# Optimization experiments

Hardware: AMD Instinct MI355X
Metric: run time of the kernel (lower is better)

Reference implementation:

```python
import jax, jax.numpy as jnp
import numpy as np

B, C, H, W = 16, 64, 128, 128
C8 = C // 8


def setup_inputs() -> dict:
    key = jax.random.key(0)
    ks = jax.random.split(key, 8)
    s = 0.05
    return {
        "x": jax.random.normal(ks[0], (B, C, H, W), dtype=jnp.float32),
        "Wq": jax.random.normal(ks[1], (C8, C), dtype=jnp.float32) * s,
        "bq": jax.random.normal(ks[2], (C8,), dtype=jnp.float32) * s,
        "Wk": jax.random.normal(ks[3], (C8, C), dtype=jnp.float32) * s,
        "bk": jax.random.normal(ks[4], (C8,), dtype=jnp.float32) * s,
        "Wv": jax.random.normal(ks[5], (C, C), dtype=jnp.float32) * s,
        "bv": jax.random.normal(ks[6], (C,), dtype=jnp.float32) * s,
        "gamma": jnp.zeros((1,), dtype=jnp.float32),
    }


def _criss_cross(x, Wq, bq, Wk, bk, Wv, bv, gamma):
    # 1x1 convs == channel-mixing matmuls
    q = jnp.einsum("bchw,oc->bohw", x, Wq) + bq[None, :, None, None]  # [B,C8,H,W]
    k = jnp.einsum("bchw,oc->bohw", x, Wk) + bk[None, :, None, None]  # [B,C8,H,W]
    v = jnp.einsum("bchw,oc->bohw", x, Wv) + bv[None, :, None, None]  # [B,C,H,W]

    h = x.shape[2]
    # column (H-axis) attention scores; diagonal masked to -inf
    energy_H = jnp.einsum("bchw,bciw->bhwi", q, k)  # [B,H,W,H]
    diag = jnp.eye(h, dtype=bool)[None, :, None, :]  # mask where query row == key row
    energy_H = jnp.where(diag, -jnp.inf, energy_H)
    # row (W-axis) attention scores
    energy_W = jnp.einsum("bchw,bchj->bhwj", q, k)  # [B,H,W,W]

    # joint softmax over concatenated H+W axis
    att = jax.nn.softmax(jnp.concatenate([energy_H, energy_W], axis=3), axis=3)
    att_H = att[:, :, :, :h]    # [B,H,W,H]
    att_W = att[:, :, :, h:]    # [B,H,W,W]

    out_H = jnp.einsum("bhwi,bciw->bchw", att_H, v)
    out_W = jnp.einsum("bhwj,bchj->bchw", att_W, v)
    return gamma[0] * (out_H + out_W) + x


def reference(x, Wq, bq, Wk, bk, Wv, bv, gamma):
    return _criss_cross(x, Wq, bq, Wk, bk, Wv, bv, gamma)
```

## Files before the change

kernel.cpp:

```cpp
#include <hip/hip_runtime.h>

#define HW 128
#define CC 64
#define C8V 8
#define NB 16
#define LOG2E 1.44269504088896f

typedef _Float16 h1;
typedef _Float16 h2 __attribute__((ext_vector_type(2)));
typedef _Float16 half8 __attribute__((ext_vector_type(8)));
typedef float float16v __attribute__((ext_vector_type(16)));
typedef uint uv4 __attribute__((ext_vector_type(4)));

__device__ __forceinline__ uint packh2(float a, float b) {
#if __has_builtin(__builtin_amdgcn_cvt_pkrtz)
  return __builtin_bit_cast(uint, __builtin_amdgcn_cvt_pkrtz(a, b));
#else
  h2 v; v[0] = (h1)a; v[1] = (h1)b; return __builtin_bit_cast(uint, v);
#endif
}
__device__ __forceinline__ ushort f2h(float a) { h1 v = (h1)a; return __builtin_bit_cast(ushort, v); }
__device__ __forceinline__ float  h2f(ushort a) { return (float)__builtin_bit_cast(h1, a); }

__device__ __forceinline__ float fexp2(float x) {
#if __has_builtin(__builtin_amdgcn_exp2f)
  return __builtin_amdgcn_exp2f(x);
#else
  return exp2f(x);
#endif
}

__device__ __forceinline__ float16v mfma16(uv4 a, uv4 b, float16v c) {
  return __builtin_amdgcn_mfma_f32_32x32x16_f16(
      __builtin_bit_cast(half8, a), __builtin_bit_cast(half8, b), c, 0, 0, 0);
}

__global__ __launch_bounds__(256) void k_proj(
    const float* __restrict__ x,
    const float* __restrict__ Wq, const float* __restrict__ bq,
    const float* __restrict__ Wk, const float* __restrict__ bk,
    const float* __restrict__ Wv, const float* __restrict__ bv,
    ushort* __restrict__ q, ushort* __restrict__ k,
    ushort* __restrict__ qT, ushort* __restrict__ kT,
    ushort* __restrict__ v)
{
  alignas(16) __shared__ ushort smem[16128];
  __shared__ float bias_l[96];
  ushort* x_l = smem;
  ushort* W_l = smem + 128 * 72;

  int t = threadIdx.x;
  int lane = t & 63, wv = t >> 6;
  int b = blockIdx.x >> 7, r = blockIdx.x & 127;

  #pragma unroll
  for (int i = 0; i < 20; ++i) {
    int idx = t + 256 * i; int o_ = idx >> 6, c = idx & 63;
    float wval = (o_ < 8) ? Wq[o_ * 64 + c] : (o_ < 16) ? Wk[(o_ - 8) * 64 + c] : Wv[(o_ - 16) * 64 + c];
    W_l[o_ * 72 + c] = f2h(wval);
  }
  if (t < 96) bias_l[t] = (t < 8) ? bq[t] : (t < 16) ? bk[t - 8] : (t < 80) ? bv[t - 16] : 0.f;

  const float* xrow = x + (size_t)(b * CC) * (HW * HW) + (size_t)r * HW;
  #pragma unroll
  for (int i = 0; i < 8; ++i) {
    int idx = t + 256 * i; int c = idx >> 5, w4 = idx & 31;
    float4 xv = *(const float4*)(xrow + (size_t)c * (HW * HW) + w4 * 4);
    x_l[(w4 * 4 + 0) * 72 + c] = f2h(xv.x);
    x_l[(w4 * 4 + 1) * 72 + c] = f2h(xv.y);
    x_l[(w4 * 4 + 2) * 72 + c] = f2h(xv.z);
    x_l[(w4 * 4 + 3) * 72 + c] = f2h(xv.w);
  }
  __syncthreads();

  int w = 32 * wv + (lane & 31);
  float16v acc0 = {}, acc1 = {}, acc2 = {};
  #pragma unroll
  for (int ks = 0; ks < 4; ++ks) {
    int c0 = 8 * (lane >> 5) + 16 * ks;
    uv4 Bx = *(const uv4*)&x_l[w * 72 + c0];
    uv4 a0 = *(const uv4*)&W_l[((lane & 31) + 0) * 72 + c0];
    uv4 a1 = *(const uv4*)&W_l[((lane & 31) + 32) * 72 + c0];
    uv4 a2 = *(const uv4*)&W_l[((lane & 31) + 64) * 72 + c0];
    acc0 = mfma16(a0, Bx, acc0);
    acc1 = mfma16(a1, Bx, acc1);
    acc2 = mfma16(a2, Bx, acc2);
  }
  __syncthreads();

  ushort* o_l  = smem;
  ushort* qk_l = smem + 8192;
  int hi = lane >> 5;

  {
    int zw = t >> 1, sel = t & 1;
    *(uv4*)&qk_l[zw * 40 + 8 + 16 * sel] = (uv4){0, 0, 0, 0};
  }

  #pragma unroll
  for (int reg = 0; reg < 16; ++reg) {
    int orow = (reg & 3) + 8 * (reg >> 2) + 4 * hi;
    float v0 = acc0[reg] + bias_l[orow];
    if (orow < 8)       qk_l[w * 40 + orow] = f2h(v0 * LOG2E);
    else if (orow < 16) qk_l[w * 40 + 8 + orow] = f2h(v0);
    else                o_l[(orow - 16) * 128 + w] = f2h(v0);
    o_l[(orow + 16) * 128 + w] = f2h(acc1[reg] + bias_l[orow + 32]);
    if (orow < 16)
      o_l[(orow + 48) * 128 + w] = f2h(acc2[reg] + bias_l[orow + 64]);
  }
  __syncthreads();

  size_t pixbase = (size_t)(b * HW + r) * HW * 16;
  {
    int pw = t >> 1, part = t & 1;
    *(uv4*)(q + pixbase + t * 8) = *(const uv4*)&qk_l[pw * 40 + part * 8];
    *(uv4*)(k + pixbase + t * 8) = *(const uv4*)&qk_l[pw * 40 + 16 + part * 8];
    size_t tbase = ((size_t)(b * HW + pw) * HW + r) * 16 + part * 8;
    *(uv4*)(qT + tbase) = *(const uv4*)&qk_l[pw * 40 + part * 8];
    *(uv4*)(kT + tbase) = *(const uv4*)&qk_l[pw * 40 + 16 + part * 8];
  }
  ushort* vb = v + (size_t)(b * CC) * (HW * HW) + (size_t)r * HW;
  #pragma unroll
  for (int i = 0; i < 4; ++i) {
    int idx = t + 256 * i; int o_ = idx >> 4, w8 = idx & 15;
    *(uv4*)(vb + (size_t)o_ * (HW * HW) + w8 * 8) = *(const uv4*)&o_l[o_ * 128 + w8 * 8];
  }
}

__global__ __launch_bounds__(256) void k_transpose_v(const ushort* __restrict__ v,
                                                     ushort* __restrict__ vT)
{
  __shared__ ushort tl[128 * 130];
  int t = threadIdx.x;
  size_t base = (size_t)blockIdx.x * (HW * HW);
  const uint* ip = (const uint*)(v + base);
  uint* op = (uint*)(vT + base);
  int c2 = t & 63;
  int r0 = t >> 6;
  for (int it = 0; it < 32; ++it) {
    int r = it * 4 + r0;
    uint val = ip[r * 64 + c2];
    *(uint*)&tl[r * 130 + c2 * 2] = val;
  }
  __syncthreads();
  for (int it = 0; it < 32; ++it) {
    int wcol = it * 4 + r0;
    int hh = c2 * 2;
    uint lo = tl[hh * 130 + wcol];
    uint hi = tl[(hh + 1) * 130 + wcol];
    op[wcol * 64 + c2] = lo | (hi << 16);
  }
}

__global__ __launch_bounds__(256, 4) void k_attn_both(
    const ushort* __restrict__ qn, const ushort* __restrict__ kn,
    const ushort* __restrict__ qT, const ushort* __restrict__ kT,
    const ushort* __restrict__ vn, const ushort* __restrict__ vT,
    ushort* __restrict__ oW_, float* __restrict__ mW_, float* __restrict__ sW_,
    ushort* __restrict__ oH_, float* __restrict__ mH_, float* __restrict__ sH_)
{
  alignas(16) __shared__ uint V_l[64 * 64];

  int t = threadIdx.x;
  int lane = t & 63, wv = t >> 6;
  int hi = lane >> 5;
  int bid = blockIdx.x & 2047;
  bool maskf = blockIdx.x >= 2048;
  const ushort* qp = maskf ? qT : qn;
  const ushort* kp = maskf ? kT : kn;
  const ushort* vp = maskf ? vT : vn;
  ushort* op = maskf ? oH_ : oW_;
  float* mo = maskf ? mH_ : mW_;
  float* so = maskf ? sH_ : sW_;

  int b = bid >> 7, r = bid & 127;
  size_t plane32 = (size_t)(HW * HW) / 2;
  size_t pixbase = (size_t)(b * HW + r) * HW * 16;

  int qg = 32 * wv + (lane & 31);
  uv4 Bq = *(const uv4*)(qp + pixbase + (size_t)qg * 16 + hi * 8);
  uv4 ka[4];
  #pragma unroll
  for (int mt = 0; mt < 4; ++mt)
    ka[mt] = *(const uv4*)(kp + pixbase + (size_t)((lane & 31) + 32 * mt) * 16 + hi * 8);

  const uint* vrow = (const uint*)vp + (size_t)(b * CC) * plane32 + (size_t)r * 64;
  #pragma unroll
  for (int i = 0; i < 4; ++i) {
    int idx = t + 256 * i; int c = idx >> 4, j4 = idx & 15;
    uv4 val = *(const uv4*)(vrow + (size_t)c * plane32 + 4 * j4);
    uint byteoff = c * 256 + ((16 * j4) ^ ((c & 15) << 4));
    *(uv4*)((char*)V_l + byteoff) = val;
  }
  __syncthreads();

  float16v e[4];
  #pragma unroll
  for (int mt = 0; mt < 4; ++mt) {
    float16v z = {};
    e[mt] = mfma16(ka[mt], Bq, z);
  }

  if (maskf) {
    #pragma unroll
    for (int mt = 0; mt < 4; ++mt)
      #pragma unroll
      for (int reg = 0; reg < 16; ++reg) {
        int key = 32 * mt + ((reg & 3) + 8 * (reg >> 2) + 4 * hi);
        e[mt][reg] = (key == qg) ? -INFINITY : e[mt][reg];
      }
  }

  float m = -INFINITY;
  #pragma unroll
  for (int mt = 0; mt < 4; ++mt)
    #pragma unroll
    for (int reg = 0; reg < 16; reg += 2)
      m = fmaxf(m, fmaxf(e[mt][reg], e[mt][reg + 1]));
  m = fmaxf(m, __shfl_xor(m, 32));

  float s0 = 0.f, s1 = 0.f, s2 = 0.f, s3 = 0.f;
  #pragma unroll
  for (int mt = 0; mt < 4; ++mt) {
    #pragma unroll
    for (int reg = 0; reg < 16; reg += 4) {
      float p0 = fexp2(e[mt][reg + 0] - m);
      float p1 = fexp2(e[mt][reg + 1] - m);
      float p2 = fexp2(e[mt][reg + 2] - m);
      float p3 = fexp2(e[mt][reg + 3] - m);
      e[mt][reg + 0] = p0; e[mt][reg + 1] = p1;
      e[mt][reg + 2] = p2; e[mt][reg + 3] = p3;
      s0 += p0; s1 += p1; s2 += p2; s3 += p3;
    }
  }
  float s = (s0 + s1) + (s2 + s3);
  s += __shfl_xor(s, 32);
  if (lane < 32) {
    mo[(size_t)bid * HW + qg] = m;
    so[(size_t)bid * HW + qg] = s;
  }

  float16v acc0 = {}, acc1 = {};
  #pragma unroll
  for (int s8 = 0; s8 < 8; ++s8) {
    int mt = s8 >> 1, hf = s8 & 1;
    float p0 = e[mt][8 * hf + 0], p1 = e[mt][8 * hf + 1];
    float p2 = e[mt][8 * hf + 2], p3 = e[mt][8 * hf + 3];
    float p4 = e[mt][8 * hf + 4], p5 = e[mt][8 * hf + 5];
    float p6 = e[mt][8 * hf + 6], p7 = e[mt][8 * hf + 7];
    uint X = packh2(p0, p1), Y = packh2(p2, p3), Z = packh2(p4, p5), Wp = packh2(p6, p7);
    uint Xs = __shfl_xor(X, 32), Ys = __shfl_xor(Y, 32);
    uint Zs = __shfl_xor(Z, 32), Ws = __shfl_xor(Wp, 32);
    uv4 Bp;
    Bp[0] = (hi == 0) ? X  : Zs;
    Bp[1] = (hi == 0) ? Y  : Ws;
    Bp[2] = (hi == 0) ? Xs : Z;
    Bp[3] = (hi == 0) ? Ys : Wp;
    #pragma unroll
    for (int ct = 0; ct < 2; ++ct) {
      int c = (lane & 31) + 32 * ct;
      uint byteoff = c * 256 + ((16 * (hi + 2 * s8)) ^ ((c & 15) << 4));
      uv4 va = *(const uv4*)((const char*)V_l + byteoff);
      if (ct == 0) acc0 = mfma16(va, Bp, acc0);
      else         acc1 = mfma16(va, Bp, acc1);
    }
  }

  __syncthreads();
  ushort* o_l = (ushort*)V_l;
  int w = 32 * wv + (lane & 31);
  #pragma unroll
  for (int reg = 0; reg < 16; ++reg) {
    int c = (reg & 3) + 8 * (reg >> 2) + 4 * hi;
    o_l[(c +  0) * 128 + w] = f2h(acc0[reg]);
    o_l[(c + 32) * 128 + w] = f2h(acc1[reg]);
  }
  __syncthreads();
  ushort* ob = op + (size_t)(b * CC) * (HW * HW) + (size_t)r * HW;
  #pragma unroll
  for (int i = 0; i < 4; ++i) {
    int idx = t + 256 * i; int c = idx >> 4, w8 = idx & 15;
    *(uv4*)(ob + (size_t)c * (HW * HW) + w8 * 8) = *(const uv4*)&o_l[c * 128 + w8 * 8];
  }
}

__global__ __launch_bounds__(256) void k_alpha(
    const float* __restrict__ mH, const float* __restrict__ sH,
    const float* __restrict__ mW, const float* __restrict__ sW,
    ushort* __restrict__ aHT, ushort* __restrict__ aWn)
{
  __shared__ float mw_l[128 * 9], sw_l[128 * 9];
  __shared__ ushort aw_l[128 * 10];
  int t = threadIdx.x;
  int b = blockIdx.x >> 4, ws = blockIdx.x & 15;
  int w0 = ws * 8;
  const int PL = HW * HW;

  #pragma unroll
  for (int i = 0; i < 4; ++i) {
    int p = t + 256 * i;
    int w = p & 7, h = p >> 3;
    mw_l[h * 9 + w] = mW[(size_t)b * PL + h * HW + w0 + w];
    sw_l[h * 9 + w] = sW[(size_t)b * PL + h * HW + w0 + w];
  }
  __syncthreads();
  #pragma unroll
  for (int i = 0; i < 4; ++i) {
    int p = t + 256 * i;
    int h = p & 127, w = p >> 7;
    size_t tidx = (size_t)b * PL + (size_t)(w0 + w) * HW + h;
    float mh = mH[tidx], sh = sH[tidx];
    float mw = mw_l[h * 9 + w], sw = sw_l[h * 9 + w];
    float mm = fmaxf(mh, mw);
    float eh = fexp2(mh - mm), ew = fexp2(mw - mm);
    float inv = 1.f / (sh * eh + sw * ew);
    aHT[tidx] = f2h(eh * inv);
    aw_l[h * 10 + w] = f2h(ew * inv);
  }
  __syncthreads();
  #pragma unroll
  for (int i = 0; i < 4; ++i) {
    int p = t + 256 * i;
    int w = p & 7, h = p >> 3;
    aWn[(size_t)b * PL + (size_t)h * HW + w0 + w] = aw_l[h * 10 + w];
  }
}

__global__ __launch_bounds__(256) void k_merge(
    const ushort* __restrict__ oHT, const ushort* __restrict__ oW,
    const ushort* __restrict__ aHT, const ushort* __restrict__ aWn,
    const float* __restrict__ x, const float* __restrict__ gamma,
    float* __restrict__ out)
{
  alignas(16) __shared__ ushort otile[2 * 32 * 132];
  int t = threadIdx.x;
  int bid = blockIdx.x;
  int wsel = bid & 3, cg = (bid >> 2) & 31, b = bid >> 7;
  int w0 = wsel * 32;
  float g = gamma[0];
  const int PL = HW * HW;

  #pragma unroll
  for (int i = 0; i < 4; ++i) {
    int p = t + 256 * i;
    int ch = p >> 9, rest = p & 511;
    int w = rest >> 4, hg = rest & 15;
    size_t cbase = (size_t)(b * CC + cg * 2 + ch) * PL;
    uv4 ov = *(const uv4*)(oHT + cbase + (size_t)(w0 + w) * HW + hg * 8);
    uv4 av = *(const uv4*)(aHT + (size_t)b * PL + (size_t)(w0 + w) * HW + hg * 8);
    uv4 res;
    #pragma unroll
    for (int jj = 0; jj < 4; ++jj) {
      h2 o2 = __builtin_bit_cast(h2, ov[jj]);
      h2 a2 = __builtin_bit_cast(h2, av[jj]);
      res[jj] = __builtin_bit_cast(uint, o2 * a2);
    }
    *(uv4*)&otile[(ch * 32 + w) * 132 + hg * 8] = res;
  }
  __syncthreads();

  #pragma unroll
  for (int ch = 0; ch < 2; ++ch) {
    size_t cbase = (size_t)(b * CC + cg * 2 + ch) * PL;
    const ushort* otc = &otile[ch * 32 * 132];
    #pragma unroll
    for (int i = 0; i < 2; ++i) {
      int p = t + 256 * i;
      int w4 = p & 7, hh2 = p >> 3;
      float th0[4], th1[4];
      #pragma unroll
      for (int j = 0; j < 4; ++j) {
        uint pk = *(const uint*)&otc[(4 * w4 + j) * 132 + 2 * hh2];
        th0[j] = h2f((ushort)(pk & 0xffff));
        th1[j] = h2f((ushort)(pk >> 16));
      }
      #pragma unroll
      for (int rr = 0; rr < 2; ++rr) {
        int hh = 2 * hh2 + rr;
        const float* th = rr ? th1 : th0;
        size_t base = cbase + (size_t)hh * HW + w0 + 4 * w4;
        size_t abase = (size_t)b * PL + (size_t)hh * HW + w0 + 4 * w4;
        uint2 aw2 = *(const uint2*)(aWn + abase);
        uint2 ow2 = *(const uint2*)(oW + base);
        float4 xv = *(const float4*)(x + base);
        float4 res;
        res.x = g * (th[0] + h2f((ushort)(ow2.x & 0xffff)) * h2f((ushort)(aw2.x & 0xffff))) + xv.x;
        res.y = g * (th[1] + h2f((ushort)(ow2.x >> 16))    * h2f((ushort)(aw2.x >> 16)))    + xv.y;
        res.z = g * (th[2] + h2f((ushort)(ow2.y & 0xffff)) * h2f((ushort)(aw2.y & 0xffff))) + xv.z;
        res.w = g * (th[3] + h2f((ushort)(ow2.y >> 16))    * h2f((ushort)(aw2.y >> 16)))    + xv.w;
        *(float4*)(out + base) = res;
      }
    }
  }
}

extern "C" void kernel_launch(void* const* d_in, const int* in_sizes, int n_in,
                              void* d_out, int out_size, void* d_ws, size_t ws_size,
                              hipStream_t stream)
{
  const float* x     = (const float*)d_in[0];
  const float* Wq    = (const float*)d_in[1];
  const float* bq    = (const float*)d_in[2];
  const float* Wk    = (const float*)d_in[3];
  const float* bk    = (const float*)d_in[4];
  const float* Wv    = (const float*)d_in[5];
  const float* bv    = (const float*)d_in[6];
  const float* gamma = (const float*)d_in[7];
  float* out = (float*)d_out;

  char* w = (char*)d_ws;
  size_t np = (size_t)NB * HW * HW;
  ushort* q   = (ushort*)w;  w += np * 16 * 2;
  ushort* k   = (ushort*)w;  w += np * 16 * 2;
  ushort* qT  = (ushort*)w;  w += np * 16 * 2;
  ushort* kT  = (ushort*)w;  w += np * 16 * 2;
  ushort* v   = (ushort*)w;  w += np * CC * 2;
  ushort* vT  = (ushort*)w;  w += np * CC * 2;
  ushort* oW  = (ushort*)w;  w += np * CC * 2;
  ushort* oHT = (ushort*)w;  w += np * CC * 2;
  float* mW = (float*)w;  w += np * 4;
  float* sW = (float*)w;  w += np * 4;
  float* mH = (float*)w;  w += np * 4;
  float* sH = (float*)w;  w += np * 4;
  ushort* aHT = (ushort*)w; w += np * 2;
  ushort* aWn = (ushort*)w; w += np * 2;
  if ((size_t)(w - (char*)d_ws) > ws_size) return;

  k_proj<<<NB * HW, 256, 0, stream>>>(x, Wq, bq, Wk, bk, Wv, bv, q, k, qT, kT, v);
  k_transpose_v<<<NB * CC, 256, 0, stream>>>(v, vT);
  k_attn_both<<<2 * NB * HW, 256, 0, stream>>>(q, k, qT, kT, v, vT,
                                               oW, mW, sW, oHT, mH, sH);
  k_alpha<<<NB * 16, 256, 0, stream>>>(mH, sH, mW, sW, aHT, aWn);
  k_merge<<<NB * 32 * 4, 256, 0, stream>>>(oHT, oW, aHT, aWn, x, gamma, out);
}
```

Measured before the change: 121.1 us.

## Prepack projection weights once, load x directly, halve q/k storage width

A new small kernel converts Wq/Wk/Wv and the biases into fp16 MFMA fragment order once, with LOG2E folded into the q weights and bias. k_proj no longer stages x and W through shared memory; each lane reads x straight from global memory and packs it into the fragment. The q/k/qT/kT buffers shrink from 16 to 8 halves per pixel, dropping the zero padding, which cuts write and read traffic. The attention kernel loads q/k only in the lower half-wave and zeroes the upper half. The trade-off is an extra kernel launch and strided scalar x loads in place of float4 loads.

```diff
diff --git a/kernel.cpp b/kernel.cpp
--- a/kernel.cpp
+++ b/kernel.cpp
@@ -35,95 +35,102 @@
       __builtin_bit_cast(half8, a), __builtin_bit_cast(half8, b), c, 0, 0, 0);
 }
 
-__global__ __launch_bounds__(256) void k_proj(
-    const float* __restrict__ x,
+__global__ __launch_bounds__(256) void k_prep(
     const float* __restrict__ Wq, const float* __restrict__ bq,
     const float* __restrict__ Wk, const float* __restrict__ bk,
     const float* __restrict__ Wv, const float* __restrict__ bv,
+    ushort* __restrict__ W_frag, float* __restrict__ bias_f)
+{
+  int idx = blockIdx.x * 256 + threadIdx.x;
+  if (idx < 6144) {
+    int g = idx >> 3, e = idx & 7;
+    int kshi = g / 96, o = g % 96;
+    int ks = kshi >> 1, hi = kshi & 1;
+    int c = 8 * hi + 16 * ks + e;
+    float val = (o < 8)  ? Wq[o * 64 + c] * LOG2E
+              : (o < 16) ? Wk[(o - 8) * 64 + c]
+              : (o < 80) ? Wv[(o - 16) * 64 + c] : 0.f;
+    W_frag[idx] = f2h(val);
+  }
+  if (blockIdx.x == 0 && threadIdx.x < 96) {
+    int t = threadIdx.x;
+    bias_f[t] = (t < 8) ? bq[t] * LOG2E : (t < 16) ? bk[t - 8] : (t < 80) ? bv[t - 16] : 0.f;
+  }
+}
+
+__global__ __launch_bounds__(256) void k_proj(
+    const float* __restrict__ x, const ushort* __restrict__ W_frag,
+    const float* __restrict__ bias_f,
     ushort* __restrict__ q, ushort* __restrict__ k,
     ushort* __restrict__ qT, ushort* __restrict__ kT,
     ushort* __restrict__ v)
 {
-  alignas(16) __shared__ ushort smem[16128];
+  alignas(16) __shared__ ushort smem[10496];
   __shared__ float bias_l[96];
-  ushort* x_l = smem;
-  ushort* W_l = smem + 128 * 72;
+  ushort* o_l  = smem;
+  ushort* qk_l = smem + 8192;
 
   int t = threadIdx.x;
-  int lane = t & 63, wv = t >> 6;
+  int lane = t & 63, wv = t >> 6, hi = lane >> 5;
   int b = blockIdx.x >> 7, r = blockIdx.x & 127;
-
-  #pragma unroll
-  for (int i = 0; i < 20; ++i) {
-    int idx = t + 256 * i; int o_ = idx >> 6, c = idx & 63;
-    float wval = (o_ < 8) ? Wq[o_ * 64 + c] : (o_ < 16) ? Wk[(o_ - 8) * 64 + c] : Wv[(o_ - 16) * 64 + c];
-    W_l[o_ * 72 + c] = f2h(wval);
-  }
-  if (t < 96) bias_l[t] = (t < 8) ? bq[t] : (t < 16) ? bk[t - 8] : (t < 80) ? bv[t - 16] : 0.f;
-
-  const float* xrow = x + (size_t)(b * CC) * (HW * HW) + (size_t)r * HW;
-  #pragma unroll
-  for (int i = 0; i < 8; ++i) {
-    int idx = t + 256 * i; int c = idx >> 5, w4 = idx & 31;
-    float4 xv = *(const float4*)(xrow + (size_t)c * (HW * HW) + w4 * 4);
-    x_l[(w4 * 4 + 0) * 72 + c] = f2h(xv.x);
-    x_l[(w4 * 4 + 1) * 72 + c] = f2h(xv.y);
-    x_l[(w4 * 4 + 2) * 72 + c] = f2h(xv.z);
-    x_l[(w4 * 4 + 3) * 72 + c] = f2h(xv.w);
-  }
-  __syncthreads();
+  if (t < 96) bias_l[t] = bias_f[t];
 
   int w = 32 * wv + (lane & 31);
+  const float* xw = x + (size_t)(b * CC) * (HW * HW) + (size_t)r * HW + w;
+  const size_t PL = (size_t)HW * HW;
+
   float16v acc0 = {}, acc1 = {}, acc2 = {};
   #pragma unroll
   for (int ks = 0; ks < 4; ++ks) {
-    int c0 = 8 * (lane >> 5) + 16 * ks;
-    uv4 Bx = *(const uv4*)&x_l[w * 72 + c0];
-    uv4 a0 = *(const uv4*)&W_l[((lane & 31) + 0) * 72 + c0];
-    uv4 a1 = *(const uv4*)&W_l[((lane & 31) + 32) * 72 + c0];
-    uv4 a2 = *(const uv4*)&W_l[((lane & 31) + 64) * 72 + c0];
+    int c0 = 8 * hi + 16 * ks;
+    uint bx[4];
+    #pragma unroll
+    for (int e2 = 0; e2 < 4; ++e2) {
+      float f0 = xw[(size_t)(c0 + 2 * e2) * PL];
+      float f1 = xw[(size_t)(c0 + 2 * e2 + 1) * PL];
+      bx[e2] = packh2(f0, f1);
+    }
+    uv4 Bx = {bx[0], bx[1], bx[2], bx[3]};
+    const ushort* wf = W_frag + (size_t)(ks * 2 + hi) * 96 * 8;
+    uv4 a0 = *(const uv4*)(wf + (lane & 31) * 8);
+    uv4 a1 = *(const uv4*)(wf + ((lane & 31) + 32) * 8);
+    uv4 a2 = *(const uv4*)(wf + ((lane & 31) + 64) * 8);
     acc0 = mfma16(a0, Bx, acc0);
     acc1 = mfma16(a1, Bx, acc1);
     acc2 = mfma16(a2, Bx, acc2);
   }
   __syncthreads();
 
-  ushort* o_l  = smem;
-  ushort* qk_l = smem + 8192;
-  int hi = lane >> 5;
-
-  {
-    int zw = t >> 1, sel = t & 1;
-    *(uv4*)&qk_l[zw * 40 + 8 + 16 * sel] = (uv4){0, 0, 0, 0};
-  }
-
   #pragma unroll
   for (int reg = 0; reg < 16; ++reg) {
     int orow = (reg & 3) + 8 * (reg >> 2) + 4 * hi;
     float v0 = acc0[reg] + bias_l[orow];
-    if (orow < 8)       qk_l[w * 40 + orow] = f2h(v0 * LOG2E);
-    else if (orow < 16) qk_l[w * 40 + 8 + orow] = f2h(v0);
-    else                o_l[(orow - 16) * 128 + w] = f2h(v0);
+    if (orow < 16) qk_l[w * 18 + orow] = f2h(v0);
+    else           o_l[(orow - 16) * 128 + w] = f2h(v0);
     o_l[(orow + 16) * 128 + w] = f2h(acc1[reg] + bias_l[orow + 32]);
     if (orow < 16)
       o_l[(orow + 48) * 128 + w] = f2h(acc2[reg] + bias_l[orow + 64]);
   }
   __syncthreads();
 
-  size_t pixbase = (size_t)(b * HW + r) * HW * 16;
   {
-    int pw = t >> 1, part = t & 1;
-    *(uv4*)(q + pixbase + t * 8) = *(const uv4*)&qk_l[pw * 40 + part * 8];
-    *(uv4*)(k + pixbase + t * 8) = *(const uv4*)&qk_l[pw * 40 + 16 + part * 8];
-    size_t tbase = ((size_t)(b * HW + pw) * HW + r) * 16 + part * 8;
-    *(uv4*)(qT + tbase) = *(const uv4*)&qk_l[pw * 40 + part * 8];
-    *(uv4*)(kT + tbase) = *(const uv4*)&qk_l[pw * 40 + 16 + part * 8];
-  }
-  ushort* vb = v + (size_t)(b * CC) * (HW * HW) + (size_t)r * HW;
+    int pix = t & 127, isk = t >> 7;
+    const ushort* src = &qk_l[pix * 18 + isk * 8];
+    uint d0 = *(const uint*)(src + 0);
+    uint d1 = *(const uint*)(src + 2);
+    uint d2 = *(const uint*)(src + 4);
+    uint d3 = *(const uint*)(src + 6);
+    uv4 val = {d0, d1, d2, d3};
+    ushort* dstn = (isk ? k : q)  + ((size_t)(b * HW + r) * HW + pix) * 8;
+    ushort* dstt = (isk ? kT : qT) + ((size_t)(b * HW + pix) * HW + r) * 8;
+    *(uv4*)dstn = val;
+    *(uv4*)dstt = val;
+  }
+  ushort* vb = v + (size_t)(b * CC) * PL + (size_t)r * HW;
   #pragma unroll
   for (int i = 0; i < 4; ++i) {
     int idx = t + 256 * i; int o_ = idx >> 4, w8 = idx & 15;
-    *(uv4*)(vb + (size_t)o_ * (HW * HW) + w8 * 8) = *(const uv4*)&o_l[o_ * 128 + w8 * 8];
+    *(uv4*)(vb + (size_t)o_ * PL + w8 * 8) = *(const uv4*)&o_l[o_ * 128 + w8 * 8];
   }
 }
 
@@ -175,14 +182,17 @@
 
   int b = bid >> 7, r = bid & 127;
   size_t plane32 = (size_t)(HW * HW) / 2;
-  size_t pixbase = (size_t)(b * HW + r) * HW * 16;
+  size_t pixbase = (size_t)(b * HW + r) * HW * 8;
 
   int qg = 32 * wv + (lane & 31);
-  uv4 Bq = *(const uv4*)(qp + pixbase + (size_t)qg * 16 + hi * 8);
-  uv4 ka[4];
-  #pragma unroll
-  for (int mt = 0; mt < 4; ++mt)
-    ka[mt] = *(const uv4*)(kp + pixbase + (size_t)((lane & 31) + 32 * mt) * 16 + hi * 8);
+  uv4 Bq = {0, 0, 0, 0};
+  uv4 ka[4] = {{0,0,0,0}, {0,0,0,0}, {0,0,0,0}, {0,0,0,0}};
+  if (hi == 0) {
+    Bq = *(const uv4*)(qp + pixbase + (size_t)qg * 8);
+    #pragma unroll
+    for (int mt = 0; mt < 4; ++mt)
+      ka[mt] = *(const uv4*)(kp + pixbase + (size_t)((lane & 31) + 32 * mt) * 8);
+  }
 
   const uint* vrow = (const uint*)vp + (size_t)(b * CC) * plane32 + (size_t)r * 64;
   #pragma unroll
@@ -410,10 +420,12 @@
 
   char* w = (char*)d_ws;
   size_t np = (size_t)NB * HW * HW;
-  ushort* q   = (ushort*)w;  w += np * 16 * 2;
-  ushort* k   = (ushort*)w;  w += np * 16 * 2;
-  ushort* qT  = (ushort*)w;  w += np * 16 * 2;
-  ushort* kT  = (ushort*)w;  w += np * 16 * 2;
+  ushort* W_frag = (ushort*)w; w += 6144 * 2;
+  float*  bias_f = (float*)w;  w += 96 * 4 + 320;
+  ushort* q   = (ushort*)w;  w += np * 8 * 2;
+  ushort* k   = (ushort*)w;  w += np * 8 * 2;
+  ushort* qT  = (ushort*)w;  w += np * 8 * 2;
+  ushort* kT  = (ushort*)w;  w += np * 8 * 2;
   ushort* v   = (ushort*)w;  w += np * CC * 2;
   ushort* vT  = (ushort*)w;  w += np * CC * 2;
   ushort* oW  = (ushort*)w;  w += np * CC * 2;
@@ -426,7 +438,8 @@
   ushort* aWn = (ushort*)w; w += np * 2;
   if ((size_t)(w - (char*)d_ws) > ws_size) return;
 
-  k_proj<<<NB * HW, 256, 0, stream>>>(x, Wq, bq, Wk, bk, Wv, bv, q, k, qT, kT, v);
+  k_prep<<<24, 256, 0, stream>>>(Wq, bq, Wk, bk, Wv, bv, W_frag, bias_f);
+  k_proj<<<NB * HW, 256, 0, stream>>>(x, W_frag, bias_f, q, k, qT, kT, v);
   k_transpose_v<<<NB * CC, 256, 0, stream>>>(v, vT);
   k_attn_both<<<2 * NB * HW, 256, 0, stream>>>(q, k, qT, kT, v, vT,
                                                oW, mW, sW, oHT, mH, sH);
```

Result: faster. 117.0 us (-3.4%).
